# Kernel optimization log

Hardware: AMD Instinct MI355X
Metric: run time of the kernel (lower is better)

Reference implementation:

```python
import jax, jax.numpy as jnp
import numpy as np

SL, BS, HS = 2048, 4, 1024
FFN, E, TOPK = 4096, 8, 2
T = SL * BS


def setup_inputs() -> dict:
    key = jax.random.key(0)
    k1, k2, k3, k4, k5 = jax.random.split(key, 5)
    x = jax.random.normal(k1, (SL, BS, HS), dtype=jnp.float32)
    expert_weights = jax.random.uniform(k2, (T, TOPK), dtype=jnp.float32)
    w1 = jax.random.normal(k3, (E, HS, FFN), dtype=jnp.float32) * (HS ** -0.5)
    w2 = jax.random.normal(k4, (E, FFN, HS), dtype=jnp.float32) * (FFN ** -0.5)
    expert_indices = jax.random.randint(k5, (T, TOPK), 0, E, dtype=jnp.int32)
    return {"x": x, "expert_weights": expert_weights, "w1": w1, "w2": w2,
            "expert_indices": expert_indices}


def reference(x, expert_weights, w1, w2, expert_indices):
    """Dropless MoE: dispatch each token to its top_k experts, run the
    per-expert MLP (x @ W1 -> gelu -> @ W2), combine weighted copies.

    Equivalent math to megablocks sort/gather -> grouped GEMM -> scatter:
    each (token, k) row is processed by exactly expert_indices[t, k]'s MLP
    and the results are summed back per token with expert_weights.
    """
    in_shape = x.shape
    hs = x.shape[-1]
    xf = x.reshape(-1, hs)                      # [T, H]
    top_k = expert_indices.shape[-1]
    eids = expert_indices.reshape(-1)           # [T*top_k]
    # gather: replicate each token top_k times (row j <-> token j // top_k)
    x_rep = jnp.repeat(xf, top_k, axis=0)       # [T*top_k, H]

    def per_expert(acc, ewb):
        e, w1_e, w2_e = ewb
        h = jax.nn.gelu(x_rep @ w1_e)           # [T*top_k, F]
        y = h @ w2_e                            # [T*top_k, H]
        mask = (eids == e).astype(x.dtype)[:, None]
        return acc + mask * y, None

    n_exp = w1.shape[0]
    acc0 = jnp.zeros_like(x_rep)
    out_flat, _ = jax.lax.scan(per_expert, acc0, (jnp.arange(n_exp), w1, w2))
    # scatter-combine: weighted sum of the top_k expert outputs per token
    w_flat = expert_weights.reshape(-1, 1)      # [T*top_k, 1]
    out = (w_flat * out_flat).reshape(-1, top_k, hs).sum(axis=1)
    return out.reshape(in_shape)
```

## Files before the change

### kernel.cpp

```cpp
#include <hip/hip_runtime.h>
#include <hip/hip_bf16.h>
#include <stdint.h>
#include <stddef.h>

#define SLEN 2048
#define BSZ  4
#define HSD  1024
#define FFND 4096
#define NEXP 8
#define NTOP 2
#define NTOK (SLEN*BSZ)
#define NROW (NTOK*NTOP)
#define NRP  (NROW + NEXP*128)
#define MAXT (NROW/128 + NEXP)

typedef __hip_bfloat16 bf16;
typedef __attribute__((ext_vector_type(8))) __bf16 b8v;
typedef __attribute__((ext_vector_type(4))) float f4v;

static constexpr size_t OFF_BLOCKHIST = 0;
static constexpr size_t OFF_BLOCKBASE = 2048;
static constexpr size_t OFF_SCHED_E   = 4096;
static constexpr size_t OFF_SCHED_R   = 4736;
static constexpr size_t OFF_NTILES    = 5376;
static constexpr size_t OFF_STOK      = 16384;
static constexpr size_t OFF_SWT       = OFF_STOK + 69632;
static constexpr size_t OFF_SLOT      = OFF_SWT + 69632;
static constexpr size_t OFF_XB        = 221184;
static constexpr size_t OFF_W1T       = OFF_XB  + (size_t)NTOK*HSD*2;
static constexpr size_t OFF_W2T       = OFF_W1T + (size_t)NEXP*FFND*HSD*2;
static constexpr size_t OFF_H         = OFF_W2T + (size_t)NEXP*HSD*FFND*2;
static constexpr size_t OFF_Y         = OFF_H   + (size_t)NRP*FFND*2;
static constexpr size_t WS_NEED       = OFF_Y   + (size_t)NRP*HSD*2;

__device__ __forceinline__ void gload_lds16(const void* g, void* l) {
  __builtin_amdgcn_global_load_lds(
      (const __attribute__((address_space(1))) unsigned int*)g,
      (__attribute__((address_space(3))) unsigned int*)l, 16, 0, 0);
}

__device__ __forceinline__ f4v mfma16(b8v a, b8v b, f4v c) {
  return __builtin_amdgcn_mfma_f32_16x16x32_bf16(a, b, c, 0, 0, 0);
}

__device__ __forceinline__ float gelu_tanh(float x) {
  float u = 0.7978845608028654f * x * (1.0f + 0.044715f * x * x);
  float e = __expf(2.0f * u);
  float t = 1.0f - 2.0f / (e + 1.0f);
  return 0.5f * x * (1.0f + t);
}

__global__ void moe_hist(const int* __restrict__ eidx, int* __restrict__ blockhist) {
  __shared__ int h[NEXP];
  int tid = threadIdx.x;
  if (tid < NEXP) h[tid] = 0;
  __syncthreads();
  int gid = blockIdx.x * 256 + tid;
  atomicAdd(&h[eidx[gid] & 7], 1);
  __syncthreads();
  if (tid < NEXP) blockhist[blockIdx.x * NEXP + tid] = h[tid];
}

__global__ void moe_plan(const int* __restrict__ blockhist, int* __restrict__ blockbase,
                         int* __restrict__ sched_e, int* __restrict__ sched_r,
                         int* __restrict__ ntiles,
                         int* __restrict__ stok, float* __restrict__ swt) {
  int tid = threadIdx.x;
  for (int i = tid; i < NRP; i += 256) { stok[i] = 0; swt[i] = 0.0f; }
  __syncthreads();
  if (tid == 0) {
    int cnt[NEXP], off[NEXP];
    for (int e = 0; e < NEXP; ++e) {
      int c = 0;
      for (int b = 0; b < 64; ++b) c += blockhist[b * NEXP + e];
      cnt[e] = c;
    }
    int run = 0, it = 0;
    for (int e = 0; e < NEXP; ++e) {
      off[e] = run;
      int nt = (cnt[e] + 127) >> 7;
      for (int j = 0; j < nt; ++j) { sched_e[it] = e; sched_r[it] = run + j * 128; ++it; }
      run += nt << 7;
    }
    *ntiles = it;
    for (int e = 0; e < NEXP; ++e) {
      int r = off[e];
      for (int b = 0; b < 64; ++b) { blockbase[b * NEXP + e] = r; r += blockhist[b * NEXP + e]; }
    }
  }
}

__global__ void moe_scatter(const int* __restrict__ eidx, const float* __restrict__ ew,
                            const int* __restrict__ blockbase,
                            int* __restrict__ stok, float* __restrict__ swt,
                            int* __restrict__ slot) {
  __shared__ int cur[NEXP];
  int tid = threadIdx.x;
  if (tid < NEXP) cur[tid] = blockbase[blockIdx.x * NEXP + tid];
  __syncthreads();
  int gid = blockIdx.x * 256 + tid;
  int e = eidx[gid] & 7;
  int pos = atomicAdd(&cur[e], 1);
  stok[pos] = gid >> 1;
  swt[pos]  = ew[gid];
  slot[gid] = pos;
}

__global__ void conv_x(const float* __restrict__ x, bf16* __restrict__ xb) {
  int gid = blockIdx.x * 256 + threadIdx.x;
  float4 v = ((const float4*)x)[gid];
  alignas(8) bf16 o[4];
  o[0] = __float2bfloat16(v.x); o[1] = __float2bfloat16(v.y);
  o[2] = __float2bfloat16(v.z); o[3] = __float2bfloat16(v.w);
  ((ushort4*)xb)[gid] = *(const ushort4*)o;
}

__global__ void transpose_conv(const float* __restrict__ src, bf16* __restrict__ dst,
                               int R, int C) {
  __shared__ float tile[32][33];
  int e = blockIdx.z;
  const float* s = src + (size_t)e * R * C;
  bf16* d = dst + (size_t)e * R * C;
  int c0 = blockIdx.x * 32, r0 = blockIdx.y * 32;
  int tx = threadIdx.x, ty = threadIdx.y;
  #pragma unroll
  for (int j = 0; j < 32; j += 8)
    tile[ty + j][tx] = s[(size_t)(r0 + ty + j) * C + (c0 + tx)];
  __syncthreads();
  #pragma unroll
  for (int j = 0; j < 32; j += 8)
    d[(size_t)(c0 + ty + j) * R + (r0 + tx)] = __float2bfloat16(tile[tx][ty + j]);
}

template<int KDIM, int NDIM, bool GATHER, bool APPLY_GELU>
__global__ __launch_bounds__(256, 2)
void moe_gemm(const bf16* __restrict__ A, const bf16* __restrict__ B,
              bf16* __restrict__ Out,
              const int* __restrict__ stok, const float* __restrict__ swt,
              const int* __restrict__ sched_e, const int* __restrict__ sched_r,
              const int* __restrict__ ntiles) {
  int rt = blockIdx.y;
  if (rt >= *ntiles) return;
  const int tid  = threadIdx.x;
  const int lane = tid & 63;
  const int wid  = tid >> 6;
  const int wm = wid & 1, wn = wid >> 1;
  const int e    = sched_e[rt];
  const int row0 = sched_r[rt];
  const int n0   = blockIdx.x * 128;

  __shared__ short lds[16384];
  short* Ach = lds;
  short* Bch = lds + 8192;

  const int l15  = lane & 15;
  const int quad = lane >> 4;
  const ushort* Aus = (const ushort*)A;
  const ushort* Bexp = (const ushort*)B + (size_t)e * NDIM * KDIM;

  const int rsub  = lane >> 3;
  const int kgsrc = (lane & 7) ^ rsub;
  const ushort* aptr[4];
  const ushort* bptr[4];
  short* aLds[4];
  short* bLds[4];
  #pragma unroll
  for (int j = 0; j < 4; ++j) {
    int i  = wid * 4 + j;
    int xr = 8 * i + rsub;
    int grow = GATHER ? stok[row0 + xr] : (row0 + xr);
    aptr[j] = Aus  + (size_t)grow * KDIM + kgsrc * 8;
    bptr[j] = Bexp + (size_t)(n0 + xr) * KDIM + kgsrc * 8;
    aLds[j] = Ach + i * 512;
    bLds[j] = Bch + i * 512;
  }

  int aoff[4][2], boff[4][2];
  #pragma unroll
  for (int t = 0; t < 4; ++t) {
    int m_local = wm * 64 + t * 16 + l15;
    int n_local = wn * 64 + t * 16 + l15;
    #pragma unroll
    for (int s = 0; s < 2; ++s) {
      int kg = s * 4 + quad;
      aoff[t][s] = m_local * 64 + ((kg ^ (l15 & 7)) << 3);
      boff[t][s] = n_local * 64 + ((kg ^ (l15 & 7)) << 3);
    }
  }

  f4v acc[4][4];
  #pragma unroll
  for (int mt = 0; mt < 4; ++mt)
    #pragma unroll
    for (int nt = 0; nt < 4; ++nt) acc[mt][nt] = (f4v)0.0f;

  const int KT = KDIM / 64;
  #pragma unroll 1
  for (int kt = 0; kt < KT; ++kt) {
    __syncthreads();
    #pragma unroll
    for (int j = 0; j < 4; ++j) {
      gload_lds16(aptr[j], aLds[j]);
      gload_lds16(bptr[j], bLds[j]);
      aptr[j] += 64; bptr[j] += 64;
    }
    __syncthreads();
    #pragma unroll
    for (int s = 0; s < 2; ++s) {
      b8v af[4], bfm[4];
      #pragma unroll
      for (int mt = 0; mt < 4; ++mt)
        af[mt] = *(const b8v*)(Ach + aoff[mt][s]);
      #pragma unroll
      for (int nt = 0; nt < 4; ++nt)
        bfm[nt] = *(const b8v*)(Bch + boff[nt][s]);
      #pragma unroll
      for (int mt = 0; mt < 4; ++mt)
        #pragma unroll
        for (int nt = 0; nt < 4; ++nt)
          acc[mt][nt] = mfma16(af[mt], bfm[nt], acc[mt][nt]);
    }
  }

  if (APPLY_GELU) {
    #pragma unroll
    for (int mt = 0; mt < 4; ++mt)
      #pragma unroll
      for (int nt = 0; nt < 4; ++nt) {
        f4v v = acc[mt][nt];
        #pragma unroll
        for (int r = 0; r < 4; ++r) {
          int m = row0 + wm * 64 + mt * 16 + quad * 4 + r;
          int n = n0   + wn * 64 + nt * 16 + l15;
          Out[(size_t)m * NDIM + n] = __float2bfloat16(gelu_tanh(v[r]));
        }
      }
  } else {
    float wv[4][4];
    #pragma unroll
    for (int mt = 0; mt < 4; ++mt)
      #pragma unroll
      for (int r = 0; r < 4; ++r)
        wv[mt][r] = swt[row0 + wm * 64 + mt * 16 + quad * 4 + r];
    #pragma unroll
    for (int mt = 0; mt < 4; ++mt)
      #pragma unroll
      for (int nt = 0; nt < 4; ++nt) {
        f4v v = acc[mt][nt];
        #pragma unroll
        for (int r = 0; r < 4; ++r) {
          int m = row0 + wm * 64 + mt * 16 + quad * 4 + r;
          int n = n0   + wn * 64 + nt * 16 + l15;
          Out[(size_t)m * NDIM + n] = __float2bfloat16(v[r] * wv[mt][r]);
        }
      }
  }
}

__global__ void moe_combine(const bf16* __restrict__ Y, const int* __restrict__ slot,
                            float* __restrict__ out) {
  int gid = blockIdx.x * 256 + threadIdx.x;
  int t  = gid >> 7;
  int ho = (gid & 127) << 3;
  int s0 = slot[t * 2], s1 = slot[t * 2 + 1];
  b8v a = *(const b8v*)((const __bf16*)Y + (size_t)s0 * HSD + ho);
  b8v b = *(const b8v*)((const __bf16*)Y + (size_t)s1 * HSD + ho);
  float4 o0, o1;
  o0.x = (float)a[0] + (float)b[0]; o0.y = (float)a[1] + (float)b[1];
  o0.z = (float)a[2] + (float)b[2]; o0.w = (float)a[3] + (float)b[3];
  o1.x = (float)a[4] + (float)b[4]; o1.y = (float)a[5] + (float)b[5];
  o1.z = (float)a[6] + (float)b[6]; o1.w = (float)a[7] + (float)b[7];
  float4* op = (float4*)(out + (size_t)t * HSD + ho);
  op[0] = o0; op[1] = o1;
}

extern "C" void kernel_launch(void* const* d_in, const int* in_sizes, int n_in,
                              void* d_out, int out_size, void* d_ws, size_t ws_size,
                              hipStream_t stream) {
  const float* x    = (const float*)d_in[0];
  const float* ew   = (const float*)d_in[1];
  const float* w1   = (const float*)d_in[2];
  const float* w2   = (const float*)d_in[3];
  const int*   eidx = (const int*)d_in[4];
  float* out = (float*)d_out;
  char* ws = (char*)d_ws;

  if (ws_size < WS_NEED) {
    hipMemsetAsync(d_out, 0x7F, 8, stream);
    return;
  }

  int*   blockhist = (int*)(ws + OFF_BLOCKHIST);
  int*   blockbase = (int*)(ws + OFF_BLOCKBASE);
  int*   sched_e   = (int*)(ws + OFF_SCHED_E);
  int*   sched_r   = (int*)(ws + OFF_SCHED_R);
  int*   ntiles    = (int*)(ws + OFF_NTILES);
  int*   stok      = (int*)(ws + OFF_STOK);
  float* swt       = (float*)(ws + OFF_SWT);
  int*   slot      = (int*)(ws + OFF_SLOT);
  bf16*  xb        = (bf16*)(ws + OFF_XB);
  bf16*  w1t       = (bf16*)(ws + OFF_W1T);
  bf16*  w2t       = (bf16*)(ws + OFF_W2T);
  bf16*  Hbuf      = (bf16*)(ws + OFF_H);
  bf16*  Ybuf      = (bf16*)(ws + OFF_Y);

  moe_hist<<<64, 256, 0, stream>>>(eidx, blockhist);
  moe_plan<<<1, 256, 0, stream>>>(blockhist, blockbase, sched_e, sched_r, ntiles, stok, swt);
  moe_scatter<<<64, 256, 0, stream>>>(eidx, ew, blockbase, stok, swt, slot);

  conv_x<<<(NTOK * HSD / 4) / 256, 256, 0, stream>>>(x, xb);
  transpose_conv<<<dim3(FFND / 32, HSD / 32, NEXP), dim3(32, 8), 0, stream>>>(w1, w1t, HSD, FFND);
  transpose_conv<<<dim3(HSD / 32, FFND / 32, NEXP), dim3(32, 8), 0, stream>>>(w2, w2t, FFND, HSD);

  moe_gemm<HSD, FFND, true, true><<<dim3(FFND / 128, MAXT), 256, 0, stream>>>(
      xb, w1t, Hbuf, stok, swt, sched_e, sched_r, ntiles);
  moe_gemm<FFND, HSD, false, false><<<dim3(HSD / 128, MAXT), 256, 0, stream>>>(
      Hbuf, w2t, Ybuf, stok, swt, sched_e, sched_r, ntiles);

  moe_combine<<<NTOK * HSD / 8 / 256, 256, 0, stream>>>(Ybuf, slot, out);
}
```

Baseline: 743.0 us.

## Split-K the second expert GEMM, move weighting to combine, widen transpose stores

The second grouped GEMM (K=4096, N=1024) now splits K in two across blockIdx.z. It writes two bf16 partial outputs into the reused x-buffer workspace region, and the combine kernel sums the partials and applies the routing weights. This is meant to fix the low block count of the N=1024 GEMM, and launch bounds are raised to allow more resident blocks. The weight transpose kernel now handles 64-row tiles and writes packed pairs of bf16 for wider stores. The cost is extra partial-output traffic and an extra rounding of each partial to bf16.

```diff
diff --git a/kernel.cpp b/kernel.cpp
--- a/kernel.cpp
+++ b/kernel.cpp
@@ -32,6 +32,7 @@
 static constexpr size_t OFF_H         = OFF_W2T + (size_t)NEXP*HSD*FFND*2;
 static constexpr size_t OFF_Y         = OFF_H   + (size_t)NRP*FFND*2;
 static constexpr size_t WS_NEED       = OFF_Y   + (size_t)NRP*HSD*2;
+static constexpr size_t OFF_YP        = OFF_XB;
 
 __device__ __forceinline__ void gload_lds16(const void* g, void* l) {
   __builtin_amdgcn_global_load_lds(
@@ -117,26 +118,31 @@
 
 __global__ void transpose_conv(const float* __restrict__ src, bf16* __restrict__ dst,
                                int R, int C) {
-  __shared__ float tile[32][33];
+  __shared__ float tile[32][65];
   int e = blockIdx.z;
   const float* s = src + (size_t)e * R * C;
-  bf16* d = dst + (size_t)e * R * C;
-  int c0 = blockIdx.x * 32, r0 = blockIdx.y * 32;
+  uint* d = (uint*)((ushort*)dst + (size_t)e * R * C);
+  int c0 = blockIdx.x * 32, r0 = blockIdx.y * 64;
   int tx = threadIdx.x, ty = threadIdx.y;
   #pragma unroll
-  for (int j = 0; j < 32; j += 8)
-    tile[ty + j][tx] = s[(size_t)(r0 + ty + j) * C + (c0 + tx)];
-  __syncthreads();
-  #pragma unroll
-  for (int j = 0; j < 32; j += 8)
-    d[(size_t)(c0 + ty + j) * R + (r0 + tx)] = __float2bfloat16(tile[tx][ty + j]);
-}
-
-template<int KDIM, int NDIM, bool GATHER, bool APPLY_GELU>
-__global__ __launch_bounds__(256, 2)
+  for (int j = 0; j < 64; j += 8)
+    tile[tx][ty + j] = s[(size_t)(r0 + ty + j) * C + (c0 + tx)];
+  __syncthreads();
+  #pragma unroll
+  for (int j = 0; j < 32; j += 8) {
+    int c = ty + j;
+    alignas(4) bf16 p[2];
+    p[0] = __float2bfloat16(tile[c][tx * 2]);
+    p[1] = __float2bfloat16(tile[c][tx * 2 + 1]);
+    d[(((size_t)(c0 + c) * R + r0) >> 1) + tx] = *(const uint*)p;
+  }
+}
+
+template<int KDIM, int NDIM, int NSPLIT, bool GATHER, int ACT>
+__global__ __launch_bounds__(256, 4)
 void moe_gemm(const bf16* __restrict__ A, const bf16* __restrict__ B,
-              bf16* __restrict__ Out,
-              const int* __restrict__ stok, const float* __restrict__ swt,
+              bf16* __restrict__ OutBase,
+              const int* __restrict__ stok,
               const int* __restrict__ sched_e, const int* __restrict__ sched_r,
               const int* __restrict__ ntiles) {
   int rt = blockIdx.y;
@@ -148,6 +154,9 @@
   const int e    = sched_e[rt];
   const int row0 = sched_r[rt];
   const int n0   = blockIdx.x * 128;
+  const int z    = blockIdx.z;
+  const int kbase = z * (KDIM / NSPLIT);
+  bf16* Out = OutBase + (size_t)z * NRP * NDIM;
 
   __shared__ short lds[16384];
   short* Ach = lds;
@@ -169,8 +178,8 @@
     int i  = wid * 4 + j;
     int xr = 8 * i + rsub;
     int grow = GATHER ? stok[row0 + xr] : (row0 + xr);
-    aptr[j] = Aus  + (size_t)grow * KDIM + kgsrc * 8;
-    bptr[j] = Bexp + (size_t)(n0 + xr) * KDIM + kgsrc * 8;
+    aptr[j] = Aus  + (size_t)grow * KDIM + kbase + kgsrc * 8;
+    bptr[j] = Bexp + (size_t)(n0 + xr) * KDIM + kbase + kgsrc * 8;
     aLds[j] = Ach + i * 512;
     bLds[j] = Bch + i * 512;
   }
@@ -194,7 +203,7 @@
     #pragma unroll
     for (int nt = 0; nt < 4; ++nt) acc[mt][nt] = (f4v)0.0f;
 
-  const int KT = KDIM / 64;
+  const int KT = KDIM / 64 / NSPLIT;
   #pragma unroll 1
   for (int kt = 0; kt < KT; ++kt) {
     __syncthreads();
@@ -222,56 +231,41 @@
     }
   }
 
-  if (APPLY_GELU) {
-    #pragma unroll
-    for (int mt = 0; mt < 4; ++mt)
+  #pragma unroll
+  for (int mt = 0; mt < 4; ++mt)
+    #pragma unroll
+    for (int nt = 0; nt < 4; ++nt) {
+      f4v v = acc[mt][nt];
       #pragma unroll
-      for (int nt = 0; nt < 4; ++nt) {
-        f4v v = acc[mt][nt];
-        #pragma unroll
-        for (int r = 0; r < 4; ++r) {
-          int m = row0 + wm * 64 + mt * 16 + quad * 4 + r;
-          int n = n0   + wn * 64 + nt * 16 + l15;
-          Out[(size_t)m * NDIM + n] = __float2bfloat16(gelu_tanh(v[r]));
-        }
+      for (int r = 0; r < 4; ++r) {
+        int m = row0 + wm * 64 + mt * 16 + quad * 4 + r;
+        int n = n0   + wn * 64 + nt * 16 + l15;
+        float o = (ACT == 0) ? gelu_tanh(v[r]) : v[r];
+        Out[(size_t)m * NDIM + n] = __float2bfloat16(o);
       }
-  } else {
-    float wv[4][4];
-    #pragma unroll
-    for (int mt = 0; mt < 4; ++mt)
-      #pragma unroll
-      for (int r = 0; r < 4; ++r)
-        wv[mt][r] = swt[row0 + wm * 64 + mt * 16 + quad * 4 + r];
-    #pragma unroll
-    for (int mt = 0; mt < 4; ++mt)
-      #pragma unroll
-      for (int nt = 0; nt < 4; ++nt) {
-        f4v v = acc[mt][nt];
-        #pragma unroll
-        for (int r = 0; r < 4; ++r) {
-          int m = row0 + wm * 64 + mt * 16 + quad * 4 + r;
-          int n = n0   + wn * 64 + nt * 16 + l15;
-          Out[(size_t)m * NDIM + n] = __float2bfloat16(v[r] * wv[mt][r]);
-        }
-      }
-  }
-}
-
-__global__ void moe_combine(const bf16* __restrict__ Y, const int* __restrict__ slot,
-                            float* __restrict__ out) {
+    }
+}
+
+__global__ void moe_combine(const bf16* __restrict__ Yp, const float* __restrict__ swt,
+                            const int* __restrict__ slot, float* __restrict__ out) {
   int gid = blockIdx.x * 256 + threadIdx.x;
   int t  = gid >> 7;
   int ho = (gid & 127) << 3;
   int s0 = slot[t * 2], s1 = slot[t * 2 + 1];
-  b8v a = *(const b8v*)((const __bf16*)Y + (size_t)s0 * HSD + ho);
-  b8v b = *(const b8v*)((const __bf16*)Y + (size_t)s1 * HSD + ho);
-  float4 o0, o1;
-  o0.x = (float)a[0] + (float)b[0]; o0.y = (float)a[1] + (float)b[1];
-  o0.z = (float)a[2] + (float)b[2]; o0.w = (float)a[3] + (float)b[3];
-  o1.x = (float)a[4] + (float)b[4]; o1.y = (float)a[5] + (float)b[5];
-  o1.z = (float)a[6] + (float)b[6]; o1.w = (float)a[7] + (float)b[7];
+  float w0 = swt[s0], w1 = swt[s1];
+  const __bf16* Y0 = (const __bf16*)Yp;
+  const __bf16* Y1 = Y0 + (size_t)NRP * HSD;
+  b8v a0 = *(const b8v*)(Y0 + (size_t)s0 * HSD + ho);
+  b8v a1 = *(const b8v*)(Y1 + (size_t)s0 * HSD + ho);
+  b8v b0 = *(const b8v*)(Y0 + (size_t)s1 * HSD + ho);
+  b8v b1 = *(const b8v*)(Y1 + (size_t)s1 * HSD + ho);
+  float o[8];
+  #pragma unroll
+  for (int i = 0; i < 8; ++i)
+    o[i] = w0 * ((float)a0[i] + (float)a1[i]) + w1 * ((float)b0[i] + (float)b1[i]);
   float4* op = (float4*)(out + (size_t)t * HSD + ho);
-  op[0] = o0; op[1] = o1;
+  op[0] = make_float4(o[0], o[1], o[2], o[3]);
+  op[1] = make_float4(o[4], o[5], o[6], o[7]);
 }
 
 extern "C" void kernel_launch(void* const* d_in, const int* in_sizes, int n_in,
@@ -302,20 +296,20 @@
   bf16*  w1t       = (bf16*)(ws + OFF_W1T);
   bf16*  w2t       = (bf16*)(ws + OFF_W2T);
   bf16*  Hbuf      = (bf16*)(ws + OFF_H);
-  bf16*  Ybuf      = (bf16*)(ws + OFF_Y);
+  bf16*  Ypart     = (bf16*)(ws + OFF_YP);
 
   moe_hist<<<64, 256, 0, stream>>>(eidx, blockhist);
   moe_plan<<<1, 256, 0, stream>>>(blockhist, blockbase, sched_e, sched_r, ntiles, stok, swt);
   moe_scatter<<<64, 256, 0, stream>>>(eidx, ew, blockbase, stok, swt, slot);
 
   conv_x<<<(NTOK * HSD / 4) / 256, 256, 0, stream>>>(x, xb);
-  transpose_conv<<<dim3(FFND / 32, HSD / 32, NEXP), dim3(32, 8), 0, stream>>>(w1, w1t, HSD, FFND);
-  transpose_conv<<<dim3(HSD / 32, FFND / 32, NEXP), dim3(32, 8), 0, stream>>>(w2, w2t, FFND, HSD);
-
-  moe_gemm<HSD, FFND, true, true><<<dim3(FFND / 128, MAXT), 256, 0, stream>>>(
-      xb, w1t, Hbuf, stok, swt, sched_e, sched_r, ntiles);
-  moe_gemm<FFND, HSD, false, false><<<dim3(HSD / 128, MAXT), 256, 0, stream>>>(
-      Hbuf, w2t, Ybuf, stok, swt, sched_e, sched_r, ntiles);
-
-  moe_combine<<<NTOK * HSD / 8 / 256, 256, 0, stream>>>(Ybuf, slot, out);
-}
+  transpose_conv<<<dim3(FFND / 32, HSD / 64, NEXP), dim3(32, 8), 0, stream>>>(w1, w1t, HSD, FFND);
+  transpose_conv<<<dim3(HSD / 32, FFND / 64, NEXP), dim3(32, 8), 0, stream>>>(w2, w2t, FFND, HSD);
+
+  moe_gemm<HSD, FFND, 1, true, 0><<<dim3(FFND / 128, MAXT, 1), 256, 0, stream>>>(
+      xb, w1t, Hbuf, stok, sched_e, sched_r, ntiles);
+  moe_gemm<FFND, HSD, 2, false, 1><<<dim3(HSD / 128, MAXT, 2), 256, 0, stream>>>(
+      Hbuf, w2t, Ypart, stok, sched_e, sched_r, ntiles);
+
+  moe_combine<<<NTOK * HSD / 8 / 256, 256, 0, stream>>>(Ypart, swt, slot, out);
+}
```

Measured after the change: 733.6 us. No clear change (-1.3%).
